# Kernel optimization log

Measured on AMD Instinct MI355X. Metric: run time of the kernel, lower is better.

Reference implementation:

```python
import jax, jax.numpy as jnp
import numpy as np

N, C, K, B, G = 32768, 128, 16, 4, 8
SCALE, BASE = 2.0, 10000.0

def _bn(x, gamma, beta, eps=1e-5):
    # torch BatchNorm1d (training): stats over all axes except channel (last)
    axes = tuple(range(x.ndim - 1))
    mean = x.mean(axes)
    var = x.var(axes)
    return (x - mean) / jnp.sqrt(var + eps) * gamma + beta

def _cayley_rope(x, coord, S_param):
    c = x.shape[-1]
    S = jnp.triu(S_param, 1)
    S = S - S.T
    I = jnp.eye(c, dtype=x.dtype)
    P = jnp.linalg.solve(I + S, I - S)  # (I+S)^-1 (I-S)
    xr = x @ P.T
    dpa = c // 3 // 2 * 2          # dim per axis (even)
    dr = dpa * 3                   # rotated dims
    inv_freq = 1.0 / (BASE ** (jnp.arange(0, dpa, 2, dtype=jnp.float32) / dpa))
    cs = coord * SCALE
    def rot(f, c1):
        ang = c1[:, None] * inv_freq[None, :]
        s, co = jnp.sin(ang), jnp.cos(ang)
        fr, fi = jnp.split(f, 2, axis=-1)
        return jnp.concatenate([fr * co - fi * s, fr * s + fi * co], -1)
    parts = [rot(xr[:, i * dpa:(i + 1) * dpa], cs[:, i]) for i in range(3)]
    out = jnp.concatenate(parts + [xr[:, dr:]], -1)
    return out @ P

def setup_inputs() -> dict:
    key = jax.random.key(0)
    ks = jax.random.split(key, 24)
    w = lambda k, i, o, s=0.02: jax.random.normal(k, (i, o), jnp.float32) * s
    inp = {
        'feat': jax.random.normal(ks[0], (N, C), jnp.float32),
        'coord': jax.random.uniform(ks[1], (N, 3), jnp.float32) * 10.0,
        'reference_index': jax.random.randint(ks[2], (N, K), 0, N),
        'offset': jnp.arange(1, B + 1, dtype=jnp.int32) * (N // B),
        'Wq': w(ks[3], C, C), 'bq': jnp.zeros((C,)),
        'gq': jnp.ones((C,)), 'bnq': jnp.zeros((C,)),
        'Wk': w(ks[4], C, C), 'bk': jnp.zeros((C,)),
        'gk': jnp.ones((C,)), 'bnk': jnp.zeros((C,)),
        'Wv': w(ks[5], C, C), 'bv': jnp.zeros((C,)),
        'S_param': jax.random.normal(ks[6], (C, C), jnp.float32) * 0.01,
        'Ww1': w(ks[7], C, G), 'bw1': jnp.zeros((G,)),
        'gw': jnp.ones((G,)), 'bnw': jnp.zeros((G,)),
        'Ww2': w(ks[8], G, G), 'bw2': jnp.zeros((G,)),
        'Wg1': w(ks[9], 2 * C, C), 'bg1': jnp.zeros((C,)),
        'gg': jnp.ones((C,)), 'bng': jnp.zeros((C,)),
        'Wg2': w(ks[10], C, G, 0.001), 'bg2': jnp.full((G,), 3.0),
    }
    return inp

def reference(feat, coord, reference_index, offset, Wq, bq, gq, bnq, Wk, bk, gk, bnk,
              Wv, bv, S_param, Ww1, bw1, gw, bnw, Ww2, bw2, Wg1, bg1, gg, bng, Wg2, bg2):
    q_raw = jax.nn.relu(_bn(feat @ Wq + bq, gq, bnq))
    k_raw = jax.nn.relu(_bn(feat @ Wk + bk, gk, bnk))
    value = feat @ Wv + bv
    q = _cayley_rope(q_raw, coord, S_param)
    k = _cayley_rope(k_raw, coord, S_param)
    kg = k[reference_index]            # [N,K,C] gather
    vg = value[reference_index]        # [N,K,C]
    rel = kg - q[:, None, :]
    geom = jax.nn.relu(_bn(rel @ Ww1 + bw1, gw, bnw)) @ Ww2 + bw2  # [N,K,G]
    seg = jnp.searchsorted(offset, jnp.arange(N), side='right')
    gmax = jax.ops.segment_max(q_raw, seg, num_segments=B)
    gate_in = jnp.concatenate([q_raw, gmax[seg]], -1)              # [N,2C]
    gate = jax.nn.sigmoid(jax.nn.relu(_bn(gate_in @ Wg1 + bg1, gg, bng)) @ Wg2 + bg2)  # [N,G]
    refined = geom * (1.0 + gate[:, None, :])
    attn = jax.nn.softmax(refined, axis=1)
    mask = jnp.sign(reference_index + 1).astype(attn.dtype)
    attn = attn * mask[:, :, None]
    vg4 = vg.reshape(N, K, G, C // G)
    out = jnp.einsum('nkgi,nkg->ngi', vg4, attn).reshape(N, C)
    return out
```

## Files before the change

kernel.cpp:

```cpp
#include <hip/hip_runtime.h>
#include <math.h>

#define N_PTS 32768
#define C_DIM 128
#define K_NB  16
#define G_DIM 8

#define OF_PW     0
#define OF_STATQ  1024
#define OF_STATK  1280
#define OF_STATG1 1536
#define OF_STATH  1792
#define OF_UMAXP  1808
#define OF_UMAXN  2320
#define OF_WQT    4096
#define OF_WKT    12288
#define OF_WVT    20480
#define OF_WG1T   28672
#define OF_PTMIT  36864
#define OF_QW     65536
#define OF_KW     327680
#define OF_GATE   589824
#define OF_G1     1048576
#define OF_V      5242880

typedef short bf16x8 __attribute__((ext_vector_type(8)));
typedef float f32x4  __attribute__((ext_vector_type(4)));

#define LSTR 136

__device__ __forceinline__ unsigned f2bf(float f) {
  unsigned u = __float_as_uint(f);
  return (u + 0x7fffu + ((u >> 16) & 1u)) >> 16;
}
__device__ __forceinline__ float bf2f(short s) {
  return __uint_as_float(((unsigned)(unsigned short)s) << 16);
}
__device__ __forceinline__ unsigned fenc(float f) {
  unsigned b = __float_as_uint(f);
  return (b & 0x80000000u) ? ~b : (b | 0x80000000u);
}
__device__ __forceinline__ float fdec(unsigned u) {
  unsigned b = (u & 0x80000000u) ? (u & 0x7fffffffu) : ~u;
  return __uint_as_float(b);
}
__device__ __forceinline__ bf16x8 pack_bf8(float4 a, float4 b) {
  bf16x8 r;
  r[0] = (short)f2bf(a.x); r[1] = (short)f2bf(a.y);
  r[2] = (short)f2bf(a.z); r[3] = (short)f2bf(a.w);
  r[4] = (short)f2bf(b.x); r[5] = (short)f2bf(b.y);
  r[6] = (short)f2bf(b.z); r[7] = (short)f2bf(b.w);
  return r;
}
__device__ __forceinline__ float fetch_asym(const float* M, int r, int c) {
  return (c > r) ? M[r*128 + c] : ((c < r) ? -M[c*128 + r] : 0.f);
}

__device__ __forceinline__ void stageB(short* dst, const short* __restrict__ src, int tid) {
  #pragma unroll
  for (int it = 0; it < 8; ++it) {
    int q = it*256 + tid;
    int r = q >> 4, c8 = q & 15;
    *(uint4*)&dst[r*LSTR + c8*8] = *(const uint4*)&src[r*128 + c8*8];
  }
}

__device__ __forceinline__ void gemm8_lds(const short* Bl, const bf16x8* af,
                                          f32x4* out, int l15, int quad)
{
  #pragma unroll
  for (int nt = 0; nt < 8; ++nt) {
    f32x4 ac = {0.f, 0.f, 0.f, 0.f};
    #pragma unroll
    for (int ks = 0; ks < 4; ++ks) {
      bf16x8 bf = *(const bf16x8*)&Bl[(nt*16 + l15)*LSTR + ks*32 + quad*8];
      ac = __builtin_amdgcn_mfma_f32_16x16x32_bf16(af[ks], bf, ac, 0, 0, 0);
    }
    out[nt] = ac;
  }
}

__global__ __launch_bounds__(256) void cayley(const float* __restrict__ Sp,
    const float* __restrict__ Ww1,
    const float* __restrict__ Wq, const float* __restrict__ Wk,
    const float* __restrict__ Wv, const float* __restrict__ Wg1,
    short* __restrict__ WqT, short* __restrict__ WkT,
    short* __restrict__ WvT, short* __restrict__ Wg1T,
    short* __restrict__ PTmIT, float* __restrict__ PW,
    float* __restrict__ statz)
{
  __shared__ short Ssh[128*LSTR];
  __shared__ float x0[128], x1[128];
  int bx = blockIdx.x, tid = threadIdx.x;
  if (bx >= 64) {
    if (bx < 80) {
      int idx = bx - 64, widx = idx >> 2, qr = idx & 3;
      const float* src = (widx == 0) ? Wq : (widx == 1) ? Wk : (widx == 2) ? Wv : Wg1;
      short* dst = (widx == 0) ? WqT : (widx == 1) ? WkT : (widx == 2) ? WvT : Wg1T;
      const float4* s4 = (const float4*)src;
      #pragma unroll
      for (int it = 0; it < 4; ++it) {
        int q = it*256 + tid; int k = qr*32 + (q >> 5), n4 = q & 31;
        float4 v = s4[k*32 + n4];
        dst[(n4*4+0)*128 + k] = (short)f2bf(v.x);
        dst[(n4*4+1)*128 + k] = (short)f2bf(v.y);
        dst[(n4*4+2)*128 + k] = (short)f2bf(v.z);
        dst[(n4*4+3)*128 + k] = (short)f2bf(v.w);
      }
    } else {
      #pragma unroll
      for (int it = 0; it < 8; ++it) {
        int idx = it*256 + tid;
        if (idx < 1808) statz[idx] = 0.f;
      }
    }
    return;
  }
  int c0 = bx*2, c1 = c0 + 1;
  #pragma unroll 8
  for (int it = 0; it < 64; ++it) {
    int idx = it*256 + tid; int i = idx >> 7, j = idx & 127;
    Ssh[i*LSTR + j] = (short)f2bf(fetch_asym(Sp, i, j));
  }
  if (tid < 128) {
    x0[tid] = (tid == c0) ? 1.f : 0.f;
    x1[tid] = (tid == c1) ? 1.f : 0.f;
  }
  __syncthreads();
  int i = tid >> 1, h = tid & 1;
  const short* srow = &Ssh[i*LSTR + h*64];
  for (int t = 0; t < 16; ++t) {
    float a0 = 0.f, a1 = 0.f;
    #pragma unroll
    for (int jq = 0; jq < 16; ++jq) {
      short4 sv = *(const short4*)&srow[jq*4];
      #pragma unroll
      for (int u = 0; u < 4; ++u) {
        float s = bf2f((&sv.x)[u]);
        int j = h*64 + jq*4 + u;
        a0 = fmaf(s, x0[j], a0);
        a1 = fmaf(s, x1[j], a1);
      }
    }
    a0 += __shfl_xor(a0, 1);
    a1 += __shfl_xor(a1, 1);
    __syncthreads();
    if (h == 0) {
      x0[i] = a0 + ((i == c0) ? 1.f : 0.f);
      x1[i] = a1 + ((i == c1) ? 1.f : 0.f);
    }
    __syncthreads();
  }
  if (tid < 128) {
    PTmIT[c0*128 + tid] = (short)f2bf(2.f*x0[tid] - ((tid == c0) ? 2.f : 0.f));
  } else {
    int t = tid - 128;
    PTmIT[c1*128 + t] = (short)f2bf(2.f*x1[t] - ((t == c1) ? 2.f : 0.f));
  }
  if (tid < 16) {
    int cc = tid >> 3, g = tid & 7;
    const float* xv = cc ? x1 : x0;
    int c = cc ? c1 : c0;
    float acc = 0.f;
    #pragma unroll 8
    for (int j = 0; j < 128; ++j) acc = fmaf(xv[j], Ww1[j*8 + g], acc);
    PW[c*8 + g] = 2.f*acc - Ww1[c*8 + g];
  }
}

__global__ __launch_bounds__(256) void qkv_mfma(const float* __restrict__ feat,
    const short* __restrict__ WqT, const short* __restrict__ WkT, const short* __restrict__ WvT,
    const float* __restrict__ bq, const float* __restrict__ bk, const float* __restrict__ bv,
    float* __restrict__ Vv,
    float* __restrict__ statq, float* __restrict__ statk,
    unsigned* __restrict__ umaxp, unsigned* __restrict__ umaxn)
{
  __shared__ short featS[64*LSTR];
  __shared__ short Bbuf[128*LSTR];
  __shared__ float ssum[2][128], ssq[2][128];
  __shared__ unsigned ump[128], umn[128];
  int tid = threadIdx.x, row0 = blockIdx.x * 64, seg = row0 >> 13;
  if (tid < 128) {
    ssum[0][tid] = 0.f; ssum[1][tid] = 0.f;
    ssq[0][tid] = 0.f;  ssq[1][tid] = 0.f;
    ump[tid] = 0u; umn[tid] = 0u;
  }
  {
    const float4* s4 = (const float4*)feat;
    #pragma unroll
    for (int it = 0; it < 8; ++it) {
      int q = it*256 + tid; int r = q >> 5, c4 = q & 31;
      float4 v = s4[(long)(row0 + r)*32 + c4];
      uint2 p;
      p.x = f2bf(v.x) | (f2bf(v.y) << 16);
      p.y = f2bf(v.z) | (f2bf(v.w) << 16);
      *(uint2*)&featS[r*LSTR + c4*4] = p;
    }
  }
  stageB(Bbuf, WqT, tid);
  __syncthreads();
  int lane = tid & 63, w = tid >> 6, l15 = lane & 15, quad = lane >> 4;
  bf16x8 af[4];
  #pragma unroll
  for (int ks = 0; ks < 4; ++ks)
    af[ks] = *(bf16x8*)&featS[(w*16 + l15)*LSTR + ks*32 + quad*8];

  {
    f32x4 acc8[8];
    gemm8_lds(Bbuf, af, acc8, l15, quad);
    #pragma unroll
    for (int nt = 0; nt < 8; ++nt) {
      int col = nt*16 + l15;
      float bb = bq[col];
      float s = 0.f, s2 = 0.f, mx = -1e30f, mn = 1e30f;
      #pragma unroll
      for (int r = 0; r < 4; ++r) {
        float v = acc8[nt][r] + bb;
        s += v; s2 = fmaf(v, v, s2); mx = fmaxf(mx, v); mn = fminf(mn, v);
      }
      s += __shfl_xor(s, 16); s += __shfl_xor(s, 32);
      s2 += __shfl_xor(s2, 16); s2 += __shfl_xor(s2, 32);
      mx = fmaxf(mx, __shfl_xor(mx, 16)); mx = fmaxf(mx, __shfl_xor(mx, 32));
      mn = fminf(mn, __shfl_xor(mn, 16)); mn = fminf(mn, __shfl_xor(mn, 32));
      if (lane < 16) {
        atomicAdd(&ssum[0][col], s); atomicAdd(&ssq[0][col], s2);
        atomicMax(&ump[col], fenc(mx)); atomicMax(&umn[col], fenc(-mn));
      }
    }
  }
  __syncthreads();
  stageB(Bbuf, WkT, tid);
  __syncthreads();
  {
    f32x4 acc8[8];
    gemm8_lds(Bbuf, af, acc8, l15, quad);
    #pragma unroll
    for (int nt = 0; nt < 8; ++nt) {
      int col = nt*16 + l15;
      float bb = bk[col];
      float s = 0.f, s2 = 0.f;
      #pragma unroll
      for (int r = 0; r < 4; ++r) {
        float v = acc8[nt][r] + bb;
        s += v; s2 = fmaf(v, v, s2);
      }
      s += __shfl_xor(s, 16); s += __shfl_xor(s, 32);
      s2 += __shfl_xor(s2, 16); s2 += __shfl_xor(s2, 32);
      if (lane < 16) { atomicAdd(&ssum[1][col], s); atomicAdd(&ssq[1][col], s2); }
    }
  }
  __syncthreads();
  stageB(Bbuf, WvT, tid);
  __syncthreads();
  {
    f32x4 acc8[8];
    gemm8_lds(Bbuf, af, acc8, l15, quad);
    #pragma unroll
    for (int nt = 0; nt < 8; ++nt) {
      int col = nt*16 + l15;
      float bb = bv[col];
      #pragma unroll
      for (int r = 0; r < 4; ++r) {
        int row = row0 + w*16 + quad*4 + r;
        Vv[(long)row*128 + col] = acc8[nt][r] + bb;
      }
    }
  }
  __syncthreads();
  if (tid < 128) {
    atomicAdd(&statq[tid], ssum[0][tid]); atomicAdd(&statq[128 + tid], ssq[0][tid]);
    atomicAdd(&statk[tid], ssum[1][tid]); atomicAdd(&statk[128 + tid], ssq[1][tid]);
    atomicMax(&umaxp[seg*128 + tid], ump[tid]);
    atomicMax(&umaxn[seg*128 + tid], umn[tid]);
  }
}

__global__ __launch_bounds__(256) void rqkw(
    const float* __restrict__ feat,
    const short* __restrict__ WqT, const short* __restrict__ WkT,
    const short* __restrict__ PTmIT, const short* __restrict__ Wg1T,
    const float* __restrict__ coord,
    const float* __restrict__ bq, const float* __restrict__ bk,
    const float* __restrict__ statq, const float* __restrict__ statk,
    const float* __restrict__ gq, const float* __restrict__ bnq,
    const float* __restrict__ gk, const float* __restrict__ bnk,
    const unsigned* __restrict__ umaxp, const unsigned* __restrict__ umaxn,
    const float* __restrict__ Wg1, const float* __restrict__ bg1,
    const float* __restrict__ PW, const float* __restrict__ bw1,
    float* __restrict__ qw, float* __restrict__ kw,
    float* __restrict__ g1, float* __restrict__ statg1)
{
  __shared__ __align__(16) char arena[60928];
  __shared__ float caq[128], cbq[128], cak[128], cbk[128];
  __shared__ float gml[128], gsg[128];
  __shared__ float ssum[128], ssq[128];
  short* featS = (short*)arena;
  short* bnqS  = (short*)(arena + 8704);
  short* bnkS  = (short*)(arena + 17408);
  short* Bbuf  = (short*)(arena + 26112);
  float* xsq = (float*)arena;
  float* xsk = (float*)(arena + 16896);
  float* pws = (float*)(arena + 33792);
  int tid = threadIdx.x;
  int row0 = blockIdx.x * 32, seg = row0 >> 13;
  const float invn = 1.f / 32768.f;
  if (tid < 128) {
    float m = statq[tid]*invn, vv = fmaf(-m, m, statq[128 + tid]*invn);
    float a = rsqrtf(vv + 1e-5f) * gq[tid];
    float b = fmaf(-m, a, bnq[tid]);
    caq[tid] = a; cbq[tid] = fmaf(a, bq[tid], b);
    float mx = fdec(umaxp[seg*128 + tid]);
    float mn = -fdec(umaxn[seg*128 + tid]);
    gml[tid] = fmaxf(0.f, fmaxf(fmaf(a, mx, b), fmaf(a, mn, b)));
    m = statk[tid]*invn; vv = fmaf(-m, m, statk[128 + tid]*invn);
    a = rsqrtf(vv + 1e-5f) * gk[tid];
    b = fmaf(-m, a, bnk[tid]);
    cak[tid] = a; cbk[tid] = fmaf(a, bk[tid], b);
    ssum[tid] = 0.f; ssq[tid] = 0.f;
  }
  {
    const float4* s4 = (const float4*)feat;
    #pragma unroll
    for (int it = 0; it < 4; ++it) {
      int q = it*256 + tid; int r = q >> 5, c4 = q & 31;
      float4 v = s4[(long)(row0 + r)*32 + c4];
      uint2 p;
      p.x = f2bf(v.x) | (f2bf(v.y) << 16);
      p.y = f2bf(v.z) | (f2bf(v.w) << 16);
      *(uint2*)&featS[r*LSTR + c4*4] = p;
    }
  }
  stageB(Bbuf, WqT, tid);
  __syncthreads();
  int lane = tid & 63, w = tid >> 6, l15 = lane & 15, quad = lane >> 4;
  bool isq = (w < 2);
  int rw = (w & 1) * 16;
  const float* ca = isq ? caq : cak;
  const float* cb = isq ? cbq : cbk;
  bf16x8 af[4];
  #pragma unroll
  for (int ks = 0; ks < 4; ++ks)
    af[ks] = *(bf16x8*)&featS[(rw + l15)*LSTR + ks*32 + quad*8];

  float bnl[32];
  if (isq) {
    f32x4 lin[8];
    gemm8_lds(Bbuf, af, lin, l15, quad);
    #pragma unroll
    for (int nt = 0; nt < 8; ++nt) {
      int col = nt*16 + l15;
      float A = ca[col], B = cb[col];
      #pragma unroll
      for (int r = 0; r < 4; ++r) {
        float v = fmaxf(0.f, fmaf(A, lin[nt][r], B));
        bnl[nt*4 + r] = v;
        bnqS[(rw + quad*4 + r)*LSTR + col] = (short)f2bf(v);
      }
    }
  }
  __syncthreads();
  stageB(Bbuf, WkT, tid);
  __syncthreads();
  if (!isq) {
    f32x4 lin[8];
    gemm8_lds(Bbuf, af, lin, l15, quad);
    #pragma unroll
    for (int nt = 0; nt < 8; ++nt) {
      int col = nt*16 + l15;
      float A = ca[col], B = cb[col];
      #pragma unroll
      for (int r = 0; r < 4; ++r) {
        float v = fmaxf(0.f, fmaf(A, lin[nt][r], B));
        bnl[nt*4 + r] = v;
        bnkS[(rw + quad*4 + r)*LSTR + col] = (short)f2bf(v);
      }
    }
  } else if (tid < 128) {
    float acc = bg1[tid];
    #pragma unroll 8
    for (int j = 0; j < 128; ++j)
      acc = fmaf(gml[j], Wg1[(128 + j)*128 + tid], acc);
    gsg[tid] = acc;
  }
  __syncthreads();
  stageB(Bbuf, PTmIT, tid);
  __syncthreads();
  bf16x8 af2[4];
  {
    const short* bnS = isq ? bnqS : bnkS;
    #pragma unroll
    for (int ks = 0; ks < 4; ++ks)
      af2[ks] = *(bf16x8*)&bnS[(rw + l15)*LSTR + ks*32 + quad*8];
  }
  f32x4 accv[8];
  gemm8_lds(Bbuf, af2, accv, l15, quad);
  __syncthreads();
  stageB(Bbuf, Wg1T, tid);
  __syncthreads();
  f32x4 accw[8];
  if (isq) gemm8_lds(Bbuf, af2, accw, l15, quad);
  __syncthreads();
  {
    float* xs = isq ? xsq : xsk;
    #pragma unroll
    for (int nt = 0; nt < 8; ++nt) {
      int col = nt*16 + l15;
      #pragma unroll
      for (int r = 0; r < 4; ++r)
        xs[(rw + quad*4 + r)*132 + col] = accv[nt][r] + bnl[nt*4 + r];
    }
  }
  #pragma unroll
  for (int it = 0; it < 4; ++it) { int idx = tid + it*256; pws[idx] = PW[idx]; }
  if (isq) {
    #pragma unroll
    for (int nt = 0; nt < 8; ++nt) {
      int col = nt*16 + l15;
      float gsv = gsg[col];
      float s = 0.f, s2 = 0.f;
      #pragma unroll
      for (int r = 0; r < 4; ++r) {
        float v = accw[nt][r] + gsv;
        int row = row0 + rw + quad*4 + r;
        g1[(long)row*128 + col] = v;
        s += v; s2 = fmaf(v, v, s2);
      }
      s += __shfl_xor(s, 16); s += __shfl_xor(s, 32);
      s2 += __shfl_xor(s2, 16); s2 += __shfl_xor(s2, 32);
      if (lane < 16) { atomicAdd(&ssum[col], s); atomicAdd(&ssq[col], s2); }
    }
  }
  __syncthreads();
  #pragma unroll
  for (int it = 0; it < 8; ++it) {
    int idx = it*256 + tid;
    int r = idx >> 6, s = idx & 63;
    if (s < 63) {
      int a3 = s / 21, j = s - a3*21;
      int cr = a3*42 + j;
      float invf = exp2f((float)(2*j) * (-13.287712379549449f / 42.f));
      float ang = coord[(row0 + r)*3 + a3] * (2.0f * invf);
      float sn, co; sincosf(ang, &sn, &co);
      float fr = xsq[r*132 + cr], fi = xsq[r*132 + cr + 21];
      xsq[r*132 + cr]      = fr*co - fi*sn;
      xsq[r*132 + cr + 21] = fr*sn + fi*co;
      fr = xsk[r*132 + cr]; fi = xsk[r*132 + cr + 21];
      xsk[r*132 + cr]      = fr*co - fi*sn;
      xsk[r*132 + cr + 21] = fr*sn + fi*co;
    }
  }
  __syncthreads();
  #pragma unroll
  for (int it = 0; it < 2; ++it) {
    int idx = it*256 + tid;
    int mat = idx >> 8, r2 = (idx >> 3) & 31, g = idx & 7;
    const float* x2 = mat ? xsk : xsq;
    float a0 = 0.f, a1 = 0.f, a2 = 0.f, a3 = 0.f;
    #pragma unroll 8
    for (int i = 0; i < 128; i += 4) {
      float4 xv = *(const float4*)&x2[r2*132 + i];
      a0 = fmaf(xv.x, pws[(i+0)*8 + g], a0);
      a1 = fmaf(xv.y, pws[(i+1)*8 + g], a1);
      a2 = fmaf(xv.z, pws[(i+2)*8 + g], a2);
      a3 = fmaf(xv.w, pws[(i+3)*8 + g], a3);
    }
    float acc = (a0 + a1) + (a2 + a3) + (mat ? bw1[g] : 0.f);
    float* dst = mat ? kw : qw;
    dst[(long)(row0 + r2)*8 + g] = acc;
  }
  if (tid < 128) {
    atomicAdd(&statg1[tid], ssum[tid]);
    atomicAdd(&statg1[128 + tid], ssq[tid]);
  }
}

__global__ __launch_bounds__(256) void mid(
    const float* __restrict__ g1, const float* __restrict__ statg1,
    const float* __restrict__ ggm, const float* __restrict__ bng,
    const float* __restrict__ Wg2, const float* __restrict__ bg2,
    float* __restrict__ gate,
    const float* __restrict__ kw, const float* __restrict__ qw,
    const int* __restrict__ ref, float* __restrict__ stath)
{
  __shared__ float gs[32][132];
  __shared__ float w2s[128][8];
  __shared__ float cA[128], cB[128];
  __shared__ float red[256];
  int tid = threadIdx.x;
  if (blockIdx.x < 1024) {
    int row0 = blockIdx.x * 32;
    #pragma unroll
    for (int it = 0; it < 4; ++it) { int idx = tid + it*256; w2s[idx >> 3][idx & 7] = Wg2[idx]; }
    if (tid < 128) {
      const float invn = 1.f / 32768.f;
      float m = statg1[tid]*invn, v = fmaf(-m, m, statg1[128 + tid]*invn);
      float a = rsqrtf(v + 1e-5f) * ggm[tid];
      cA[tid] = a; cB[tid] = fmaf(-m, a, bng[tid]);
    }
    #pragma unroll
    for (int it = 0; it < 4; ++it) {
      int idx = tid + it*256; int r = idx >> 5, cq = idx & 31;
      *(float4*)&gs[r][cq*4] = *(const float4*)&g1[(long)(row0 + r)*128 + cq*4];
    }
    __syncthreads();
    int r = tid >> 3, g = tid & 7;
    float acc = bg2[g];
    #pragma unroll 8
    for (int c2 = 0; c2 < 128; ++c2) {
      float act = fmaxf(0.f, fmaf(gs[r][c2], cA[c2], cB[c2]));
      acc = fmaf(act, w2s[c2][g], acc);
    }
    gate[(long)(row0 + r)*8 + g] = 1.f / (1.f + expf(-acc));
  } else {
    long base = (long)(blockIdx.x - 1024) * 4096;
    float s = 0.f, sq = 0.f;
    for (int it = 0; it < 16; ++it) {
      long idx = base + it*256 + tid;
      int n = (int)(idx >> 7); int kk = (int)((idx >> 3) & 15); int g = (int)(idx & 7);
      int r = ref[n*16 + kk];
      float h = kw[(long)r*8 + g] - qw[(long)n*8 + g];
      s += h; sq = fmaf(h, h, sq);
    }
    red[tid] = s; __syncthreads();
    for (int d = 128; d >= 8; d >>= 1) { if (tid < d) red[tid] += red[tid + d]; __syncthreads(); }
    if (tid < 8) atomicAdd(&stath[tid], red[tid]);
    __syncthreads();
    red[tid] = sq; __syncthreads();
    for (int d = 128; d >= 8; d >>= 1) { if (tid < d) red[tid] += red[tid + d]; __syncthreads(); }
    if (tid < 8) atomicAdd(&stath[8 + tid], red[tid]);
  }
}

__global__ __launch_bounds__(256) void attn_out(const float* __restrict__ qw, const float* __restrict__ kw,
                                                const float* __restrict__ stath,
                                                const float* __restrict__ gw, const float* __restrict__ bnw,
                                                const float* __restrict__ Ww2, const float* __restrict__ bw2,
                                                const float* __restrict__ gate, const int* __restrict__ ref,
                                                const float* __restrict__ v, float* __restrict__ out)
{
  __shared__ float sm1[2][16][9];
  __shared__ float sm2[2][16][9];
  __shared__ int   smr[2][16];
  int tid = threadIdx.x; int rh = tid >> 7, t = tid & 127;
  int n = blockIdx.x * 2 + rh;
  int kk = t >> 3, g = t & 7;
  if (t < 16) smr[rh][t] = ref[n*16 + t];
  __syncthreads();
  const float invnk = 1.f / 524288.f;
  float m0 = stath[g]*invnk, v0 = fmaf(-m0, m0, stath[8 + g]*invnk);
  float aw = rsqrtf(v0 + 1e-5f) * gw[g];
  float bw = fmaf(-m0, aw, bnw[g]);
  int rr = smr[rh][kk];
  float h = kw[(long)rr*8 + g] - qw[(long)n*8 + g];
  sm1[rh][kk][g] = fmaxf(0.f, fmaf(h, aw, bw));
  __syncthreads();
  float acc = bw2[g];
  #pragma unroll
  for (int g2 = 0; g2 < 8; ++g2) acc = fmaf(sm1[rh][kk][g2], Ww2[g2*8 + g], acc);
  float refined = acc * (1.f + gate[(long)n*8 + g]);
  sm2[rh][kk][g] = refined;
  __syncthreads();
  float mx = -1e30f;
  #pragma unroll
  for (int k2 = 0; k2 < 16; ++k2) mx = fmaxf(mx, sm2[rh][k2][g]);
  float e = expf(refined - mx);
  sm1[rh][kk][g] = e;
  __syncthreads();
  float ssum = 0.f;
  #pragma unroll
  for (int k2 = 0; k2 < 16; ++k2) ssum += sm1[rh][k2][g];
  float mask = ((rr + 1) > 0) ? 1.f : (((rr + 1) == 0) ? 0.f : -1.f);
  float attn = e / ssum * mask;
  sm2[rh][kk][g] = attn;
  __syncthreads();
  float o = 0.f;
  #pragma unroll
  for (int k2 = 0; k2 < 16; ++k2) {
    o = fmaf(v[(long)smr[rh][k2]*128 + t], sm2[rh][k2][t >> 4], o);
  }
  out[(long)n*128 + t] = o;
}

extern "C" void kernel_launch(void* const* d_in, const int* in_sizes, int n_in,
                              void* d_out, int out_size, void* d_ws, size_t ws_size,
                              hipStream_t stream)
{
  const float* feat  = (const float*)d_in[0];
  const float* coord = (const float*)d_in[1];
  const int*   ref   = (const int*)d_in[2];
  const float* Wq  = (const float*)d_in[4];
  const float* bq  = (const float*)d_in[5];
  const float* gq  = (const float*)d_in[6];
  const float* bnq = (const float*)d_in[7];
  const float* Wk  = (const float*)d_in[8];
  const float* bk  = (const float*)d_in[9];
  const float* gk  = (const float*)d_in[10];
  const float* bnk = (const float*)d_in[11];
  const float* Wv  = (const float*)d_in[12];
  const float* bv  = (const float*)d_in[13];
  const float* Sp  = (const float*)d_in[14];
  const float* Ww1 = (const float*)d_in[15];
  const float* bw1 = (const float*)d_in[16];
  const float* gw  = (const float*)d_in[17];
  const float* bnw = (const float*)d_in[18];
  const float* Ww2 = (const float*)d_in[19];
  const float* bw2 = (const float*)d_in[20];
  const float* Wg1 = (const float*)d_in[21];
  const float* bg1 = (const float*)d_in[22];
  const float* ggm = (const float*)d_in[23];
  const float* bng = (const float*)d_in[24];
  const float* Wg2 = (const float*)d_in[25];
  const float* bg2 = (const float*)d_in[26];
  float* out = (float*)d_out;

  float* W = (float*)d_ws;
  float* PW = W + OF_PW;
  short* WqT   = (short*)(W + OF_WQT);
  short* WkT   = (short*)(W + OF_WKT);
  short* WvT   = (short*)(W + OF_WVT);
  short* Wg1T  = (short*)(W + OF_WG1T);
  short* PTmIT = (short*)(W + OF_PTMIT);
  float* G1 = W + OF_G1;
  float* Vv = W + OF_V;

  cayley<<<81, 256, 0, stream>>>(Sp, Ww1, Wq, Wk, Wv, Wg1,
                                 WqT, WkT, WvT, Wg1T, PTmIT, PW, W + OF_STATQ);
  qkv_mfma<<<512, 256, 0, stream>>>(feat, WqT, WkT, WvT, bq, bk, bv, Vv,
                                    W + OF_STATQ, W + OF_STATK,
                                    (unsigned*)(W + OF_UMAXP), (unsigned*)(W + OF_UMAXN));
  rqkw<<<1024, 256, 0, stream>>>(feat, WqT, WkT, PTmIT, Wg1T, coord,
                                 bq, bk,
                                 W + OF_STATQ, W + OF_STATK,
                                 gq, bnq, gk, bnk,
                                 (const unsigned*)(W + OF_UMAXP), (const unsigned*)(W + OF_UMAXN),
                                 Wg1, bg1, PW, bw1,
                                 W + OF_QW, W + OF_KW, G1, W + OF_STATG1);
  mid<<<2048, 256, 0, stream>>>(G1, W + OF_STATG1, ggm, bng, Wg2, bg2, W + OF_GATE,
                                W + OF_KW, W + OF_QW, ref, W + OF_STATH);
  attn_out<<<16384, 256, 0, stream>>>(W + OF_QW, W + OF_KW, W + OF_STATH, gw, bnw, Ww2, bw2,
                                      W + OF_GATE, ref, Vv, out);
}
```

Before: 315.5 us.

## Store linear Q/K projections in qkv pass and read B operands directly from global

The QKV kernel now writes the pre-bias Q and K projections to scratch buffers (reusing the output buffer and the G1 region). rqkw then reads these instead of recomputing the feat@Wq/Wk GEMMs. Weight B-fragments are read straight from global/L2 instead of being staged through LDS, which drops several syncthreads and shrinks LDS use, with higher occupancy hints. The work is re-split so each wave computes either Q or K plus a quarter of V over 32-row blocks. The trade-off is extra global write and read traffic of two N×C float tensors, plus aliasing of the output and G1 buffers that the later kernels must respect.

```diff
diff --git a/kernel.cpp b/kernel.cpp
--- a/kernel.cpp
+++ b/kernel.cpp
@@ -56,16 +56,7 @@
   return (c > r) ? M[r*128 + c] : ((c < r) ? -M[c*128 + r] : 0.f);
 }
 
-__device__ __forceinline__ void stageB(short* dst, const short* __restrict__ src, int tid) {
-  #pragma unroll
-  for (int it = 0; it < 8; ++it) {
-    int q = it*256 + tid;
-    int r = q >> 4, c8 = q & 15;
-    *(uint4*)&dst[r*LSTR + c8*8] = *(const uint4*)&src[r*128 + c8*8];
-  }
-}
-
-__device__ __forceinline__ void gemm8_lds(const short* Bl, const bf16x8* af,
+__device__ __forceinline__ void gemm8_glb(const short* __restrict__ Bg, const bf16x8* af,
                                           f32x4* out, int l15, int quad)
 {
   #pragma unroll
@@ -73,7 +64,7 @@
     f32x4 ac = {0.f, 0.f, 0.f, 0.f};
     #pragma unroll
     for (int ks = 0; ks < 4; ++ks) {
-      bf16x8 bf = *(const bf16x8*)&Bl[(nt*16 + l15)*LSTR + ks*32 + quad*8];
+      bf16x8 bf = *(const bf16x8*)&Bg[(nt*16 + l15)*128 + ks*32 + quad*8];
       ac = __builtin_amdgcn_mfma_f32_16x16x32_bf16(af[ks], bf, ac, 0, 0, 0);
     }
     out[nt] = ac;
@@ -168,102 +159,82 @@
   }
 }
 
-__global__ __launch_bounds__(256) void qkv_mfma(const float* __restrict__ feat,
+__global__ __launch_bounds__(256, 4) void qkv_mfma(const float* __restrict__ feat,
     const short* __restrict__ WqT, const short* __restrict__ WkT, const short* __restrict__ WvT,
     const float* __restrict__ bq, const float* __restrict__ bk, const float* __restrict__ bv,
-    float* __restrict__ Vv,
+    float* __restrict__ Vv, float* __restrict__ Qlin, float* Klin,
     float* __restrict__ statq, float* __restrict__ statk,
     unsigned* __restrict__ umaxp, unsigned* __restrict__ umaxn)
 {
-  __shared__ short featS[64*LSTR];
-  __shared__ short Bbuf[128*LSTR];
   __shared__ float ssum[2][128], ssq[2][128];
   __shared__ unsigned ump[128], umn[128];
-  int tid = threadIdx.x, row0 = blockIdx.x * 64, seg = row0 >> 13;
+  int tid = threadIdx.x, row0 = blockIdx.x * 32, seg = row0 >> 13;
   if (tid < 128) {
     ssum[0][tid] = 0.f; ssum[1][tid] = 0.f;
     ssq[0][tid] = 0.f;  ssq[1][tid] = 0.f;
     ump[tid] = 0u; umn[tid] = 0u;
   }
+  int lane = tid & 63, w = tid >> 6, l15 = lane & 15, quad = lane >> 4;
+  int rw = (w & 1) * 16;
+  bool isq = (w < 2);
+  bf16x8 af[4];
   {
-    const float4* s4 = (const float4*)feat;
-    #pragma unroll
-    for (int it = 0; it < 8; ++it) {
-      int q = it*256 + tid; int r = q >> 5, c4 = q & 31;
-      float4 v = s4[(long)(row0 + r)*32 + c4];
-      uint2 p;
-      p.x = f2bf(v.x) | (f2bf(v.y) << 16);
-      p.y = f2bf(v.z) | (f2bf(v.w) << 16);
-      *(uint2*)&featS[r*LSTR + c4*4] = p;
-    }
-  }
-  stageB(Bbuf, WqT, tid);
-  __syncthreads();
-  int lane = tid & 63, w = tid >> 6, l15 = lane & 15, quad = lane >> 4;
-  bf16x8 af[4];
-  #pragma unroll
-  for (int ks = 0; ks < 4; ++ks)
-    af[ks] = *(bf16x8*)&featS[(w*16 + l15)*LSTR + ks*32 + quad*8];
-
+    long rbase = (long)(row0 + rw + l15) * 128;
+    #pragma unroll
+    for (int ks = 0; ks < 4; ++ks) {
+      int c0 = ks*32 + quad*8;
+      float4 v0 = *(const float4*)&feat[rbase + c0];
+      float4 v1 = *(const float4*)&feat[rbase + c0 + 4];
+      af[ks] = pack_bf8(v0, v1);
+    }
+  }
+  __syncthreads();
   {
+    const short* Wqk = isq ? WqT : WkT;
+    const float* bqk = isq ? bq : bk;
+    float* linD = isq ? Qlin : Klin;
+    int si = isq ? 0 : 1;
     f32x4 acc8[8];
-    gemm8_lds(Bbuf, af, acc8, l15, quad);
+    gemm8_glb(Wqk, af, acc8, l15, quad);
     #pragma unroll
     for (int nt = 0; nt < 8; ++nt) {
       int col = nt*16 + l15;
-      float bb = bq[col];
+      float bb = bqk[col];
       float s = 0.f, s2 = 0.f, mx = -1e30f, mn = 1e30f;
       #pragma unroll
       for (int r = 0; r < 4; ++r) {
-        float v = acc8[nt][r] + bb;
+        float raw = acc8[nt][r];
+        linD[(long)(row0 + rw + quad*4 + r)*128 + col] = raw;
+        float v = raw + bb;
         s += v; s2 = fmaf(v, v, s2); mx = fmaxf(mx, v); mn = fminf(mn, v);
       }
       s += __shfl_xor(s, 16); s += __shfl_xor(s, 32);
       s2 += __shfl_xor(s2, 16); s2 += __shfl_xor(s2, 32);
-      mx = fmaxf(mx, __shfl_xor(mx, 16)); mx = fmaxf(mx, __shfl_xor(mx, 32));
-      mn = fminf(mn, __shfl_xor(mn, 16)); mn = fminf(mn, __shfl_xor(mn, 32));
+      if (isq) {
+        mx = fmaxf(mx, __shfl_xor(mx, 16)); mx = fmaxf(mx, __shfl_xor(mx, 32));
+        mn = fminf(mn, __shfl_xor(mn, 16)); mn = fminf(mn, __shfl_xor(mn, 32));
+      }
       if (lane < 16) {
-        atomicAdd(&ssum[0][col], s); atomicAdd(&ssq[0][col], s2);
-        atomicMax(&ump[col], fenc(mx)); atomicMax(&umn[col], fenc(-mn));
-      }
-    }
-  }
-  __syncthreads();
-  stageB(Bbuf, WkT, tid);
-  __syncthreads();
+        atomicAdd(&ssum[si][col], s); atomicAdd(&ssq[si][col], s2);
+        if (isq) { atomicMax(&ump[col], fenc(mx)); atomicMax(&umn[col], fenc(-mn)); }
+      }
+    }
+  }
   {
-    f32x4 acc8[8];
-    gemm8_lds(Bbuf, af, acc8, l15, quad);
-    #pragma unroll
-    for (int nt = 0; nt < 8; ++nt) {
-      int col = nt*16 + l15;
-      float bb = bk[col];
-      float s = 0.f, s2 = 0.f;
-      #pragma unroll
-      for (int r = 0; r < 4; ++r) {
-        float v = acc8[nt][r] + bb;
-        s += v; s2 = fmaf(v, v, s2);
-      }
-      s += __shfl_xor(s, 16); s += __shfl_xor(s, 32);
-      s2 += __shfl_xor(s2, 16); s2 += __shfl_xor(s2, 32);
-      if (lane < 16) { atomicAdd(&ssum[1][col], s); atomicAdd(&ssq[1][col], s2); }
-    }
-  }
-  __syncthreads();
-  stageB(Bbuf, WvT, tid);
-  __syncthreads();
-  {
-    f32x4 acc8[8];
-    gemm8_lds(Bbuf, af, acc8, l15, quad);
-    #pragma unroll
-    for (int nt = 0; nt < 8; ++nt) {
-      int col = nt*16 + l15;
+    int ntb = (w >> 1) * 4;
+    #pragma unroll
+    for (int nt = 0; nt < 4; ++nt) {
+      f32x4 ac = {0.f, 0.f, 0.f, 0.f};
+      #pragma unroll
+      for (int ks = 0; ks < 4; ++ks) {
+        bf16x8 bf = *(const bf16x8*)&WvT[((ntb + nt)*16 + l15)*128 + ks*32 + quad*8];
+        ac = __builtin_amdgcn_mfma_f32_16x16x32_bf16(af[ks], bf, ac, 0, 0, 0);
+      }
+      int col = (ntb + nt)*16 + l15;
       float bb = bv[col];
       #pragma unroll
-      for (int r = 0; r < 4; ++r) {
-        int row = row0 + w*16 + quad*4 + r;
-        Vv[(long)row*128 + col] = acc8[nt][r] + bb;
-      }
+      for (int r = 0; r < 4; ++r)
+        Vv[(long)(row0 + rw + quad*4 + r)*128 + col] = ac[r] + bb;
     }
   }
   __syncthreads();
@@ -275,9 +246,8 @@
   }
 }
 
-__global__ __launch_bounds__(256) void rqkw(
-    const float* __restrict__ feat,
-    const short* __restrict__ WqT, const short* __restrict__ WkT,
+__global__ __launch_bounds__(256, 3) void rqkw(
+    const float* __restrict__ qlin, const float* klin,
     const short* __restrict__ PTmIT, const short* __restrict__ Wg1T,
     const float* __restrict__ coord,
     const float* __restrict__ bq, const float* __restrict__ bk,
@@ -288,16 +258,12 @@
     const float* __restrict__ Wg1, const float* __restrict__ bg1,
     const float* __restrict__ PW, const float* __restrict__ bw1,
     float* __restrict__ qw, float* __restrict__ kw,
-    float* __restrict__ g1, float* __restrict__ statg1)
-{
-  __shared__ __align__(16) char arena[60928];
+    float* g1, float* __restrict__ statg1)
+{
+  __shared__ __align__(16) char arena[37888];
   __shared__ float caq[128], cbq[128], cak[128], cbk[128];
   __shared__ float gml[128], gsg[128];
   __shared__ float ssum[128], ssq[128];
-  short* featS = (short*)arena;
-  short* bnqS  = (short*)(arena + 8704);
-  short* bnkS  = (short*)(arena + 17408);
-  short* Bbuf  = (short*)(arena + 26112);
   float* xsq = (float*)arena;
   float* xsk = (float*)(arena + 16896);
   float* pws = (float*)(arena + 33792);
@@ -318,100 +284,67 @@
     cak[tid] = a; cbk[tid] = fmaf(a, bk[tid], b);
     ssum[tid] = 0.f; ssq[tid] = 0.f;
   }
-  {
-    const float4* s4 = (const float4*)feat;
-    #pragma unroll
-    for (int it = 0; it < 4; ++it) {
-      int q = it*256 + tid; int r = q >> 5, c4 = q & 31;
-      float4 v = s4[(long)(row0 + r)*32 + c4];
-      uint2 p;
-      p.x = f2bf(v.x) | (f2bf(v.y) << 16);
-      p.y = f2bf(v.z) | (f2bf(v.w) << 16);
-      *(uint2*)&featS[r*LSTR + c4*4] = p;
-    }
-  }
-  stageB(Bbuf, WqT, tid);
+  #pragma unroll
+  for (int it = 0; it < 4; ++it) { int idx = it*256 + tid; pws[idx] = PW[idx]; }
   __syncthreads();
   int lane = tid & 63, w = tid >> 6, l15 = lane & 15, quad = lane >> 4;
   bool isq = (w < 2);
   int rw = (w & 1) * 16;
   const float* ca = isq ? caq : cak;
   const float* cb = isq ? cbq : cbk;
-  bf16x8 af[4];
-  #pragma unroll
-  for (int ks = 0; ks < 4; ++ks)
-    af[ks] = *(bf16x8*)&featS[(rw + l15)*LSTR + ks*32 + quad*8];
-
+  const float* lin = isq ? qlin : klin;
+  bf16x8 af2[4];
+  #pragma unroll
+  for (int ks = 0; ks < 4; ++ks) {
+    int c0 = ks*32 + quad*8;
+    const float* lp = &lin[(long)(row0 + rw + l15)*128 + c0];
+    float4 v0 = *(const float4*)lp;
+    float4 v1 = *(const float4*)(lp + 4);
+    float4 b0, b1;
+    b0.x = fmaxf(0.f, fmaf(ca[c0+0], v0.x, cb[c0+0]));
+    b0.y = fmaxf(0.f, fmaf(ca[c0+1], v0.y, cb[c0+1]));
+    b0.z = fmaxf(0.f, fmaf(ca[c0+2], v0.z, cb[c0+2]));
+    b0.w = fmaxf(0.f, fmaf(ca[c0+3], v0.w, cb[c0+3]));
+    b1.x = fmaxf(0.f, fmaf(ca[c0+4], v1.x, cb[c0+4]));
+    b1.y = fmaxf(0.f, fmaf(ca[c0+5], v1.y, cb[c0+5]));
+    b1.z = fmaxf(0.f, fmaf(ca[c0+6], v1.z, cb[c0+6]));
+    b1.w = fmaxf(0.f, fmaf(ca[c0+7], v1.w, cb[c0+7]));
+    af2[ks] = pack_bf8(b0, b1);
+  }
+  f32x4 accv[8];
+  gemm8_glb(PTmIT, af2, accv, l15, quad);
+  f32x4 accw[8];
+  if (isq) {
+    gemm8_glb(Wg1T, af2, accw, l15, quad);
+  } else {
+    int c = tid - 128;
+    float acc = bg1[c];
+    #pragma unroll 8
+    for (int j = 0; j < 128; ++j)
+      acc = fmaf(gml[j], Wg1[(128 + j)*128 + c], acc);
+    gsg[c] = acc;
+  }
   float bnl[32];
-  if (isq) {
-    f32x4 lin[8];
-    gemm8_lds(Bbuf, af, lin, l15, quad);
+  #pragma unroll
+  for (int nt = 0; nt < 8; ++nt) {
+    int col = nt*16 + l15;
+    float A = ca[col], B = cb[col];
+    long rb = (long)(row0 + rw + quad*4)*128 + col;
+    #pragma unroll
+    for (int r = 0; r < 4; ++r)
+      bnl[nt*4 + r] = fmaxf(0.f, fmaf(A, lin[rb + (long)r*128], B));
+  }
+  __syncthreads();
+  {
+    float* xs = isq ? xsq : xsk;
     #pragma unroll
     for (int nt = 0; nt < 8; ++nt) {
       int col = nt*16 + l15;
-      float A = ca[col], B = cb[col];
-      #pragma unroll
-      for (int r = 0; r < 4; ++r) {
-        float v = fmaxf(0.f, fmaf(A, lin[nt][r], B));
-        bnl[nt*4 + r] = v;
-        bnqS[(rw + quad*4 + r)*LSTR + col] = (short)f2bf(v);
-      }
-    }
-  }
-  __syncthreads();
-  stageB(Bbuf, WkT, tid);
-  __syncthreads();
-  if (!isq) {
-    f32x4 lin[8];
-    gemm8_lds(Bbuf, af, lin, l15, quad);
-    #pragma unroll
-    for (int nt = 0; nt < 8; ++nt) {
-      int col = nt*16 + l15;
-      float A = ca[col], B = cb[col];
-      #pragma unroll
-      for (int r = 0; r < 4; ++r) {
-        float v = fmaxf(0.f, fmaf(A, lin[nt][r], B));
-        bnl[nt*4 + r] = v;
-        bnkS[(rw + quad*4 + r)*LSTR + col] = (short)f2bf(v);
-      }
-    }
-  } else if (tid < 128) {
-    float acc = bg1[tid];
-    #pragma unroll 8
-    for (int j = 0; j < 128; ++j)
-      acc = fmaf(gml[j], Wg1[(128 + j)*128 + tid], acc);
-    gsg[tid] = acc;
-  }
-  __syncthreads();
-  stageB(Bbuf, PTmIT, tid);
-  __syncthreads();
-  bf16x8 af2[4];
-  {
-    const short* bnS = isq ? bnqS : bnkS;
-    #pragma unroll
-    for (int ks = 0; ks < 4; ++ks)
-      af2[ks] = *(bf16x8*)&bnS[(rw + l15)*LSTR + ks*32 + quad*8];
-  }
-  f32x4 accv[8];
-  gemm8_lds(Bbuf, af2, accv, l15, quad);
-  __syncthreads();
-  stageB(Bbuf, Wg1T, tid);
-  __syncthreads();
-  f32x4 accw[8];
-  if (isq) gemm8_lds(Bbuf, af2, accw, l15, quad);
-  __syncthreads();
-  {
-    float* xs = isq ? xsq : xsk;
-    #pragma unroll
-    for (int nt = 0; nt < 8; ++nt) {
-      int col = nt*16 + l15;
       #pragma unroll
       for (int r = 0; r < 4; ++r)
         xs[(rw + quad*4 + r)*132 + col] = accv[nt][r] + bnl[nt*4 + r];
     }
   }
-  #pragma unroll
-  for (int it = 0; it < 4; ++it) { int idx = tid + it*256; pws[idx] = PW[idx]; }
   if (isq) {
     #pragma unroll
     for (int nt = 0; nt < 8; ++nt) {
@@ -421,8 +354,7 @@
       #pragma unroll
       for (int r = 0; r < 4; ++r) {
         float v = accw[nt][r] + gsv;
-        int row = row0 + rw + quad*4 + r;
-        g1[(long)row*128 + col] = v;
+        g1[(long)(row0 + rw + quad*4 + r)*128 + col] = v;
         s += v; s2 = fmaf(v, v, s2);
       }
       s += __shfl_xor(s, 16); s += __shfl_xor(s, 32);
@@ -431,6 +363,10 @@
     }
   }
   __syncthreads();
+  if (tid < 128) {
+    atomicAdd(&statg1[tid], ssum[tid]);
+    atomicAdd(&statg1[128 + tid], ssq[tid]);
+  }
   #pragma unroll
   for (int it = 0; it < 8; ++it) {
     int idx = it*256 + tid;
@@ -467,10 +403,6 @@
     float acc = (a0 + a1) + (a2 + a3) + (mat ? bw1[g] : 0.f);
     float* dst = mat ? kw : qw;
     dst[(long)(row0 + r2)*8 + g] = acc;
-  }
-  if (tid < 128) {
-    atomicAdd(&statg1[tid], ssum[tid]);
-    atomicAdd(&statg1[128 + tid], ssq[tid]);
   }
 }
 
@@ -622,13 +554,16 @@
   short* PTmIT = (short*)(W + OF_PTMIT);
   float* G1 = W + OF_G1;
   float* Vv = W + OF_V;
+  float* Qlin = (float*)d_out;
+  float* Klin = G1;
 
   cayley<<<81, 256, 0, stream>>>(Sp, Ww1, Wq, Wk, Wv, Wg1,
                                  WqT, WkT, WvT, Wg1T, PTmIT, PW, W + OF_STATQ);
-  qkv_mfma<<<512, 256, 0, stream>>>(feat, WqT, WkT, WvT, bq, bk, bv, Vv,
-                                    W + OF_STATQ, W + OF_STATK,
-                                    (unsigned*)(W + OF_UMAXP), (unsigned*)(W + OF_UMAXN));
-  rqkw<<<1024, 256, 0, stream>>>(feat, WqT, WkT, PTmIT, Wg1T, coord,
+  qkv_mfma<<<1024, 256, 0, stream>>>(feat, WqT, WkT, WvT, bq, bk, bv, Vv,
+                                     Qlin, Klin,
+                                     W + OF_STATQ, W + OF_STATK,
+                                     (unsigned*)(W + OF_UMAXP), (unsigned*)(W + OF_UMAXN));
+  rqkw<<<1024, 256, 0, stream>>>(Qlin, Klin, PTmIT, Wg1T, coord,
                                  bq, bk,
                                  W + OF_STATQ, W + OF_STATK,
                                  gq, bnq, gk, bnk,
```

Result: slower. 354.5 us (+12.4%).

## Stage weight tiles via async global-to-LDS loads with XOR swizzle and double buffering

Applied to the files above, without the earlier changes.

Weight-tile staging now uses `__builtin_amdgcn_global_load_lds` (16-byte direct global-to-LDS copies) into unpadded tiles, and the MFMA B-fragment reads use an XOR swizzle on the row to avoid bank conflicts. In `qkv_mfma` the next weight matrix is loaded into a second LDS buffer while the current GEMM runs, and the feature rows go straight from global memory into registers. Together these remove the register round-trip through VGPRs, several barriers and the padded LDS layout. The per-segment max/min tracking now uses pre-bias values, with the bias folded back in downstream. The change relies on `__syncthreads` waiting for outstanding async LDS writes, and on the swizzle applied at load time matching the one used at read time.

```diff
diff --git a/kernel.cpp b/kernel.cpp
--- a/kernel.cpp
+++ b/kernel.cpp
@@ -56,28 +56,32 @@
   return (c > r) ? M[r*128 + c] : ((c < r) ? -M[c*128 + r] : 0.f);
 }
 
-__device__ __forceinline__ void stageB(short* dst, const short* __restrict__ src, int tid) {
+__device__ __forceinline__ void g2l16(const void* g, void* l) {
+  __builtin_amdgcn_global_load_lds(
+      (const __attribute__((address_space(1))) void*)g,
+      (__attribute__((address_space(3))) void*)l, 16, 0, 0);
+}
+
+__device__ __forceinline__ void stage_async(short* dst, const short* __restrict__ src, int tid) {
+  int lane = tid & 63, wv = tid >> 6;
   #pragma unroll
   for (int it = 0; it < 8; ++it) {
-    int q = it*256 + tid;
-    int r = q >> 4, c8 = q & 15;
-    *(uint4*)&dst[r*LSTR + c8*8] = *(const uint4*)&src[r*128 + c8*8];
-  }
-}
-
-__device__ __forceinline__ void gemm8_lds(const short* Bl, const bf16x8* af,
-                                          f32x4* out, int l15, int quad)
-{
-  #pragma unroll
-  for (int nt = 0; nt < 8; ++nt) {
-    f32x4 ac = {0.f, 0.f, 0.f, 0.f};
-    #pragma unroll
-    for (int ks = 0; ks < 4; ++ks) {
-      bf16x8 bf = *(const bf16x8*)&Bl[(nt*16 + l15)*LSTR + ks*32 + quad*8];
-      ac = __builtin_amdgcn_mfma_f32_16x16x32_bf16(af[ks], bf, ac, 0, 0, 0);
-    }
-    out[nt] = ac;
-  }
+    int chunk = it*256 + wv*64;
+    int D = (chunk + lane)*16;
+    int gs = D ^ (((D >> 8) & 7) << 4);
+    g2l16((const char*)src + gs, (char*)dst + chunk*16);
+  }
+}
+
+__device__ __forceinline__ f32x4 mfma1(const short* Bb, const bf16x8* a4, int row, int quad) {
+  f32x4 ac = {0.f, 0.f, 0.f, 0.f};
+  int sx = (row & 7) << 4;
+  #pragma unroll
+  for (int ks = 0; ks < 4; ++ks) {
+    const char* p = (const char*)Bb + (((row*256) + ks*64 + quad*16) ^ sx);
+    ac = __builtin_amdgcn_mfma_f32_16x16x32_bf16(a4[ks], *(const bf16x8*)p, ac, 0, 0, 0);
+  }
+  return ac;
 }
 
 __global__ __launch_bounds__(256) void cayley(const float* __restrict__ Sp,
@@ -168,55 +172,51 @@
   }
 }
 
-__global__ __launch_bounds__(256) void qkv_mfma(const float* __restrict__ feat,
+__global__ __launch_bounds__(256, 2) void qkv_mfma(const float* __restrict__ feat,
     const short* __restrict__ WqT, const short* __restrict__ WkT, const short* __restrict__ WvT,
     const float* __restrict__ bq, const float* __restrict__ bk, const float* __restrict__ bv,
     float* __restrict__ Vv,
     float* __restrict__ statq, float* __restrict__ statk,
     unsigned* __restrict__ umaxp, unsigned* __restrict__ umaxn)
 {
-  __shared__ short featS[64*LSTR];
-  __shared__ short Bbuf[128*LSTR];
+  __shared__ __align__(16) short Bb0[128*128];
+  __shared__ __align__(16) short Bb1[128*128];
   __shared__ float ssum[2][128], ssq[2][128];
   __shared__ unsigned ump[128], umn[128];
   int tid = threadIdx.x, row0 = blockIdx.x * 64, seg = row0 >> 13;
+  int lane = tid & 63, w = tid >> 6, l15 = lane & 15, quad = lane >> 4;
+  stage_async(Bb0, WqT, tid);
   if (tid < 128) {
     ssum[0][tid] = 0.f; ssum[1][tid] = 0.f;
     ssq[0][tid] = 0.f;  ssq[1][tid] = 0.f;
     ump[tid] = 0u; umn[tid] = 0u;
   }
+  bf16x8 af[4];
   {
-    const float4* s4 = (const float4*)feat;
-    #pragma unroll
-    for (int it = 0; it < 8; ++it) {
-      int q = it*256 + tid; int r = q >> 5, c4 = q & 31;
-      float4 v = s4[(long)(row0 + r)*32 + c4];
-      uint2 p;
-      p.x = f2bf(v.x) | (f2bf(v.y) << 16);
-      p.y = f2bf(v.z) | (f2bf(v.w) << 16);
-      *(uint2*)&featS[r*LSTR + c4*4] = p;
-    }
-  }
-  stageB(Bbuf, WqT, tid);
-  __syncthreads();
-  int lane = tid & 63, w = tid >> 6, l15 = lane & 15, quad = lane >> 4;
-  bf16x8 af[4];
-  #pragma unroll
-  for (int ks = 0; ks < 4; ++ks)
-    af[ks] = *(bf16x8*)&featS[(w*16 + l15)*LSTR + ks*32 + quad*8];
-
+    long rbase = (long)(row0 + w*16 + l15) * 128;
+    #pragma unroll
+    for (int ks = 0; ks < 4; ++ks) {
+      int c0 = ks*32 + quad*8;
+      float4 v0 = *(const float4*)&feat[rbase + c0];
+      float4 v1 = *(const float4*)&feat[rbase + c0 + 4];
+      af[ks] = pack_bf8(v0, v1);
+    }
+  }
+  __syncthreads();
+  stage_async(Bb1, WkT, tid);
   {
-    f32x4 acc8[8];
-    gemm8_lds(Bbuf, af, acc8, l15, quad);
     #pragma unroll
     for (int nt = 0; nt < 8; ++nt) {
+      f32x4 ac = mfma1(Bb0, af, nt*16 + l15, quad);
       int col = nt*16 + l15;
       float bb = bq[col];
       float s = 0.f, s2 = 0.f, mx = -1e30f, mn = 1e30f;
       #pragma unroll
       for (int r = 0; r < 4; ++r) {
-        float v = acc8[nt][r] + bb;
-        s += v; s2 = fmaf(v, v, s2); mx = fmaxf(mx, v); mn = fminf(mn, v);
+        float raw = ac[r];
+        float v = raw + bb;
+        s += v; s2 = fmaf(v, v, s2);
+        mx = fmaxf(mx, raw); mn = fminf(mn, raw);
       }
       s += __shfl_xor(s, 16); s += __shfl_xor(s, 32);
       s2 += __shfl_xor(s2, 16); s2 += __shfl_xor(s2, 32);
@@ -229,19 +229,17 @@
     }
   }
   __syncthreads();
-  stageB(Bbuf, WkT, tid);
-  __syncthreads();
+  stage_async(Bb0, WvT, tid);
   {
-    f32x4 acc8[8];
-    gemm8_lds(Bbuf, af, acc8, l15, quad);
     #pragma unroll
     for (int nt = 0; nt < 8; ++nt) {
+      f32x4 ac = mfma1(Bb1, af, nt*16 + l15, quad);
       int col = nt*16 + l15;
       float bb = bk[col];
       float s = 0.f, s2 = 0.f;
       #pragma unroll
       for (int r = 0; r < 4; ++r) {
-        float v = acc8[nt][r] + bb;
+        float v = ac[r] + bb;
         s += v; s2 = fmaf(v, v, s2);
       }
       s += __shfl_xor(s, 16); s += __shfl_xor(s, 32);
@@ -250,20 +248,15 @@
     }
   }
   __syncthreads();
-  stageB(Bbuf, WvT, tid);
-  __syncthreads();
   {
-    f32x4 acc8[8];
-    gemm8_lds(Bbuf, af, acc8, l15, quad);
     #pragma unroll
     for (int nt = 0; nt < 8; ++nt) {
+      f32x4 ac = mfma1(Bb0, af, nt*16 + l15, quad);
       int col = nt*16 + l15;
       float bb = bv[col];
       #pragma unroll
-      for (int r = 0; r < 4; ++r) {
-        int row = row0 + w*16 + quad*4 + r;
-        Vv[(long)row*128 + col] = acc8[nt][r] + bb;
-      }
+      for (int r = 0; r < 4; ++r)
+        Vv[(long)(row0 + w*16 + quad*4 + r)*128 + col] = ac[r] + bb;
     }
   }
   __syncthreads();
@@ -290,7 +283,7 @@
     float* __restrict__ qw, float* __restrict__ kw,
     float* __restrict__ g1, float* __restrict__ statg1)
 {
-  __shared__ __align__(16) char arena[60928];
+  __shared__ __align__(16) char arena[58880];
   __shared__ float caq[128], cbq[128], cak[128], cbk[128];
   __shared__ float gml[128], gsg[128];
   __shared__ float ssum[128], ssq[128];
@@ -304,14 +297,16 @@
   int tid = threadIdx.x;
   int row0 = blockIdx.x * 32, seg = row0 >> 13;
   const float invn = 1.f / 32768.f;
+  stage_async(Bbuf, WqT, tid);
   if (tid < 128) {
     float m = statq[tid]*invn, vv = fmaf(-m, m, statq[128 + tid]*invn);
     float a = rsqrtf(vv + 1e-5f) * gq[tid];
     float b = fmaf(-m, a, bnq[tid]);
-    caq[tid] = a; cbq[tid] = fmaf(a, bq[tid], b);
+    float cb2 = fmaf(a, bq[tid], b);
+    caq[tid] = a; cbq[tid] = cb2;
     float mx = fdec(umaxp[seg*128 + tid]);
     float mn = -fdec(umaxn[seg*128 + tid]);
-    gml[tid] = fmaxf(0.f, fmaxf(fmaf(a, mx, b), fmaf(a, mn, b)));
+    gml[tid] = fmaxf(0.f, fmaxf(fmaf(a, mx, cb2), fmaf(a, mn, cb2)));
     m = statk[tid]*invn; vv = fmaf(-m, m, statk[128 + tid]*invn);
     a = rsqrtf(vv + 1e-5f) * gk[tid];
     b = fmaf(-m, a, bnk[tid]);
@@ -330,7 +325,6 @@
       *(uint2*)&featS[r*LSTR + c4*4] = p;
     }
   }
-  stageB(Bbuf, WqT, tid);
   __syncthreads();
   int lane = tid & 63, w = tid >> 6, l15 = lane & 15, quad = lane >> 4;
   bool isq = (w < 2);
@@ -344,33 +338,31 @@
 
   float bnl[32];
   if (isq) {
-    f32x4 lin[8];
-    gemm8_lds(Bbuf, af, lin, l15, quad);
     #pragma unroll
     for (int nt = 0; nt < 8; ++nt) {
+      f32x4 ac = mfma1(Bbuf, af, nt*16 + l15, quad);
       int col = nt*16 + l15;
       float A = ca[col], B = cb[col];
       #pragma unroll
       for (int r = 0; r < 4; ++r) {
-        float v = fmaxf(0.f, fmaf(A, lin[nt][r], B));
+        float v = fmaxf(0.f, fmaf(A, ac[r], B));
         bnl[nt*4 + r] = v;
         bnqS[(rw + quad*4 + r)*LSTR + col] = (short)f2bf(v);
       }
     }
   }
   __syncthreads();
-  stageB(Bbuf, WkT, tid);
+  stage_async(Bbuf, WkT, tid);
   __syncthreads();
   if (!isq) {
-    f32x4 lin[8];
-    gemm8_lds(Bbuf, af, lin, l15, quad);
     #pragma unroll
     for (int nt = 0; nt < 8; ++nt) {
+      f32x4 ac = mfma1(Bbuf, af, nt*16 + l15, quad);
       int col = nt*16 + l15;
       float A = ca[col], B = cb[col];
       #pragma unroll
       for (int r = 0; r < 4; ++r) {
-        float v = fmaxf(0.f, fmaf(A, lin[nt][r], B));
+        float v = fmaxf(0.f, fmaf(A, ac[r], B));
         bnl[nt*4 + r] = v;
         bnkS[(rw + quad*4 + r)*LSTR + col] = (short)f2bf(v);
       }
@@ -383,8 +375,7 @@
     gsg[tid] = acc;
   }
   __syncthreads();
-  stageB(Bbuf, PTmIT, tid);
-  __syncthreads();
+  stage_async(Bbuf, PTmIT, tid);
   bf16x8 af2[4];
   {
     const short* bnS = isq ? bnqS : bnkS;
@@ -392,13 +383,20 @@
     for (int ks = 0; ks < 4; ++ks)
       af2[ks] = *(bf16x8*)&bnS[(rw + l15)*LSTR + ks*32 + quad*8];
   }
+  __syncthreads();
   f32x4 accv[8];
-  gemm8_lds(Bbuf, af2, accv, l15, quad);
-  __syncthreads();
-  stageB(Bbuf, Wg1T, tid);
+  #pragma unroll
+  for (int nt = 0; nt < 8; ++nt)
+    accv[nt] = mfma1(Bbuf, af2, nt*16 + l15, quad);
+  __syncthreads();
+  stage_async(Bbuf, Wg1T, tid);
   __syncthreads();
   f32x4 accw[8];
-  if (isq) gemm8_lds(Bbuf, af2, accw, l15, quad);
+  if (isq) {
+    #pragma unroll
+    for (int nt = 0; nt < 8; ++nt)
+      accw[nt] = mfma1(Bbuf, af2, nt*16 + l15, quad);
+  }
   __syncthreads();
   {
     float* xs = isq ? xsq : xsk;
```

After: 316.9 us. No clear change (+0.4%).
